# Kernel optimization log

Measured on AMD Instinct MI355X. Metric: run time of the kernel, lower is better.

Reference implementation:

```python
import jax, jax.numpy as jnp
import numpy as np

D_HEAD = 64
KV_GROUPS = 3
KSIZE = 7


def _win_idx(L, ksize):
    # NATTEN neighborhood: window centered at i, shifted to stay in-bounds.
    start = jnp.clip(jnp.arange(L) - ksize // 2, 0, L - ksize)  # [L]
    return start[:, None] + jnp.arange(ksize)[None, :]          # [L, k]


def _natten2d(q, k, v, ksize):
    # q,k,v: [n, nh, H, W, e]; q pre-scaled.
    H, W = q.shape[2], q.shape[3]
    ih = _win_idx(H, ksize)  # [H, k]
    iw = _win_idx(W, ksize)  # [W, k]
    # gather per-query key/value windows: [n, nh, H, W, k, k, e]
    kg = k[:, :, ih[:, None, :, None], iw[None, :, None, :], :]
    vg = v[:, :, ih[:, None, :, None], iw[None, :, None, :], :]
    logits = jnp.einsum('nhije,nhijabe->nhijab', q, kg)  # [n,nh,H,W,k,k]
    n_, nh = logits.shape[:2]
    a = jax.nn.softmax(logits.reshape(n_, nh, H, W, ksize * ksize), axis=-1)
    a = a.reshape(logits.shape)
    return jnp.einsum('nhijab,nhijabe->nhije', a, vg)  # [n,nh,H,W,e]


def _to_heads(p, nh, e):
    n, h, w, _ = p.shape
    return p.reshape(n, h, w, nh, e).transpose(0, 3, 1, 2, 4)  # [n,nh,h,w,e]


def setup_inputs() -> dict:
    key = jax.random.key(0)
    k1, k2, k3 = jax.random.split(key, 3)
    x = jax.random.normal(k1, (2, 32, 32, 768), dtype=jnp.float32)
    w_qkv = jax.random.normal(k2, (1280, 768), dtype=jnp.float32) * 0.02
    w_out = jax.random.normal(k3, (768, 768), dtype=jnp.float32) * 0.02
    return {"x": x, "w_qkv": w_qkv, "w_out": w_out}


def reference(x, w_qkv, w_out):
    n, H, W, d_model = x.shape
    q_heads = d_model // D_HEAD
    kv_heads = q_heads // KV_GROUPS
    qkv = x @ w_qkv.T  # [n,H,W,1280]
    q, k, v = jnp.split(
        qkv, [q_heads * D_HEAD, (q_heads + kv_heads) * D_HEAD], axis=-1)
    q = _to_heads(q, q_heads, D_HEAD)
    k = jnp.tile(_to_heads(k, kv_heads, D_HEAD), (1, KV_GROUPS, 1, 1, 1))
    v = jnp.tile(_to_heads(v, kv_heads, D_HEAD), (1, KV_GROUPS, 1, 1, 1))
    q = q / (D_HEAD ** 0.5)
    o = _natten2d(q, k, v, KSIZE)           # [n,nh,H,W,e]
    o = o.transpose(0, 2, 3, 1, 4).reshape(n, H, W, d_model)
    return o @ w_out.T
```

## Files before the change

kernel.cpp:

```cpp
#include <hip/hip_runtime.h>
#include <hip/hip_bf16.h>


typedef __attribute__((ext_vector_type(8))) __bf16 bf16x8;
typedef __attribute__((ext_vector_type(4))) float floatx4;
typedef unsigned short u16;

__device__ inline u16 f2bf(float f) {
    union { float f; unsigned u; } v; v.f = f;
    return (u16)((v.u + 0x7fff + ((v.u >> 16) & 1)) >> 16);
}

__device__ inline void gl_lds16(const void* g, void* l) {
    __builtin_amdgcn_global_load_lds(
        (const __attribute__((address_space(1))) void*)g,
        (__attribute__((address_space(3))) void*)l, 16, 0, 0);
}

__global__ __launch_bounds__(256) void convert_kernel(
    const float* __restrict__ x, const float* __restrict__ w1,
    const float* __restrict__ w2, u16* __restrict__ xb,
    u16* __restrict__ w1b, u16* __restrict__ w2b)
{
    int t = blockIdx.x * blockDim.x + threadIdx.x;
    const float* s; u16* d;
    if (t < 393216)      { s = x;  d = xb; }
    else if (t < 638976) { s = w1; d = w1b; t -= 393216; }
    else                 { s = w2; d = w2b; t -= 638976; }
    float4 v = ((const float4*)s)[t];
    ushort4 o;
    o.x = f2bf(v.x); o.y = f2bf(v.y); o.z = f2bf(v.z); o.w = f2bf(v.w);
    ((ushort4*)d)[t] = o;
}

template<int MODE>
__global__ __launch_bounds__(256) void gemm_nt(
    const u16* __restrict__ A, const u16* __restrict__ B,
    float* __restrict__ out, u16* __restrict__ Cq, u16* __restrict__ vT,
    int K)
{
    __shared__ __align__(16) u16 As[8 * 2048];
    __shared__ __align__(16) u16 Bs[8 * 2048];
    const int tid = threadIdx.x;
    const int lane = tid & 63;
    const int wave = tid >> 6;
    const int bm = blockIdx.y * 64;
    const int bn = blockIdx.x * 64;
    const int qr = (wave >> 1) * 32;
    const int qc = (wave & 1) * 32;

    floatx4 acc[2][2] = {};

    const u16* Xsrc = (wave < 2) ? A : B;
    const int   bx  = (wave < 2) ? bm : bn;
    u16* Xlds       = (wave < 2) ? As : Bs;
    const int half  = wave & 1;
    const int l2 = lane >> 2;
    const int l3 = (lane & 3) * 8;
    int gofs[16], lofs[16];
    #pragma unroll
    for (int cc = 0; cc < 16; cc++) {
        int c = half * 16 + cc, kc = c & 7, rg = c >> 3;
        gofs[cc] = (bx + rg * 16 + l2) * K + kc * 32 + l3;
        lofs[cc] = kc * 2048 + rg * 512;
    }

    const int fr = lane & 15;
    const int fk = (lane >> 4) * 8;

    for (int k0 = 0; k0 < K; k0 += 256) {
        #pragma unroll
        for (int cc = 0; cc < 16; cc++)
            gl_lds16(Xsrc + gofs[cc] + k0, Xlds + lofs[cc]);
        __syncthreads();
        #pragma unroll
        for (int kc = 0; kc < 8; kc++) {
            bf16x8 af0 = *(const bf16x8*)&As[kc * 2048 + (qr +      fr) * 32 + fk];
            bf16x8 af1 = *(const bf16x8*)&As[kc * 2048 + (qr + 16 + fr) * 32 + fk];
            bf16x8 bf0 = *(const bf16x8*)&Bs[kc * 2048 + (qc +      fr) * 32 + fk];
            bf16x8 bf1 = *(const bf16x8*)&Bs[kc * 2048 + (qc + 16 + fr) * 32 + fk];
            acc[0][0] = __builtin_amdgcn_mfma_f32_16x16x32_bf16(af0, bf0, acc[0][0], 0, 0, 0);
            acc[0][1] = __builtin_amdgcn_mfma_f32_16x16x32_bf16(af0, bf1, acc[0][1], 0, 0, 0);
            acc[1][0] = __builtin_amdgcn_mfma_f32_16x16x32_bf16(af1, bf0, acc[1][0], 0, 0, 0);
            acc[1][1] = __builtin_amdgcn_mfma_f32_16x16x32_bf16(af1, bf1, acc[1][1], 0, 0, 0);
        }
        __syncthreads();
    }

    const int cr = (lane >> 4) * 4;
    const int ccol = lane & 15;
    #pragma unroll
    for (int i = 0; i < 2; i++) {
        #pragma unroll
        for (int j = 0; j < 2; j++) {
            const int row0 = bm + qr + i * 16 + cr;
            const int col  = bn + qc + j * 16 + ccol;
            if (MODE == 0) {
                float4 w = {acc[i][j][0], acc[i][j][1], acc[i][j][2], acc[i][j][3]};
                *(float4*)&out[(size_t)col * 768 + row0] = w;
            } else {
                if (row0 < 1024) {
                    ushort4 w;
                    w.x = f2bf(acc[i][j][0]); w.y = f2bf(acc[i][j][1]);
                    w.z = f2bf(acc[i][j][2]); w.w = f2bf(acc[i][j][3]);
                    *(ushort4*)&Cq[(size_t)col * 1024 + row0] = w;
                } else {
                    #pragma unroll
                    for (int r = 0; r < 4; r++)
                        vT[(size_t)(row0 + r - 1024) * 2048 + col] = f2bf(acc[i][j][r]);
                }
            }
        }
    }
}

__global__ __launch_bounds__(256) void natten_mfma(
    const u16* __restrict__ qkv, const u16* __restrict__ vT,
    u16* __restrict__ o)
{
    __shared__ __align__(16) u16 Pw[4 * 512];
    const int h  = blockIdx.x;
    const int tb = blockIdx.y;
    const int g  = h & 3;
    const int batch = tb >> 4;
    const int ti = ((tb >> 2) & 3) * 8;
    const int tj = (tb & 3) * 8;
    const int wu_i = min(max(ti - 3, 0), 18);
    const int oj   = min(max(tj - 3, 0) & ~3, 16);
    const int lane = threadIdx.x & 63, wave = threadIdx.x >> 6;
    const int pixbase = batch << 10;

    const int fr = lane & 15;
    const int fk = (lane >> 4) * 8;

    bf16x8 aq0, aq1;
    {
        int qq = wave * 16 + fr;
        int pixq = pixbase + (ti + (qq >> 3)) * 32 + tj + (qq & 7);
        const u16* qp = &qkv[(size_t)pixq * 1024 + h * 64];
        aq0 = *(const bf16x8*)(qp + fk);
        aq1 = *(const bf16x8*)(qp + 32 + fk);
    }

    bool colok[4]; int tlo[4], thi[4];
    #pragma unroll
    for (int r = 0; r < 4; r++) {
        int qq = wave * 16 + (lane >> 4) * 4 + r;
        int qi = ti + (qq >> 3), qj = tj + (qq & 7);
        int si = min(max(qi - 3, 0), 25);
        int sj = min(max(qj - 3, 0), 25);
        colok[r] = (oj + fr >= sj) && (oj + fr <= sj + 6);
        tlo[r] = si - wu_i; thi[r] = tlo[r] + 6;
    }

    float s[14][4];
    float mx[4] = {-1e30f, -1e30f, -1e30f, -1e30f};
    #pragma unroll
    for (int t = 0; t < 14; t++) {
        int kp = pixbase + (wu_i + t) * 32 + oj + fr;
        const u16* krow = &qkv[(size_t)kp * 1024 + 768 + g * 64];
        bf16x8 bk0 = *(const bf16x8*)(krow + fk);
        bf16x8 bk1 = *(const bf16x8*)(krow + 32 + fk);
        floatx4 a4 = {};
        a4 = __builtin_amdgcn_mfma_f32_16x16x32_bf16(aq0, bk0, a4, 0, 0, 0);
        a4 = __builtin_amdgcn_mfma_f32_16x16x32_bf16(aq1, bk1, a4, 0, 0, 0);
        #pragma unroll
        for (int r = 0; r < 4; r++) {
            bool v = colok[r] && (t >= tlo[r]) && (t <= thi[r]);
            s[t][r] = v ? a4[r] * 0.125f : -1e30f;
            mx[r] = fmaxf(mx[r], s[t][r]);
        }
    }
    #pragma unroll
    for (int r = 0; r < 4; r++) {
        mx[r] = fmaxf(mx[r], __shfl_xor(mx[r], 1));
        mx[r] = fmaxf(mx[r], __shfl_xor(mx[r], 2));
        mx[r] = fmaxf(mx[r], __shfl_xor(mx[r], 4));
        mx[r] = fmaxf(mx[r], __shfl_xor(mx[r], 8));
    }
    float l[4] = {0.f, 0.f, 0.f, 0.f};
    #pragma unroll
    for (int t = 0; t < 14; t++)
        #pragma unroll
        for (int r = 0; r < 4; r++) {
            float p = __expf(s[t][r] - mx[r]);
            s[t][r] = p; l[r] += p;
        }
    #pragma unroll
    for (int r = 0; r < 4; r++) {
        l[r] += __shfl_xor(l[r], 1);
        l[r] += __shfl_xor(l[r], 2);
        l[r] += __shfl_xor(l[r], 4);
        l[r] += __shfl_xor(l[r], 8);
    }
    float rinv[4];
    #pragma unroll
    for (int r = 0; r < 4; r++) rinv[r] = 1.0f / l[r];

    u16* pw = &Pw[wave * 512];
    floatx4 oacc[4] = {};
    const int vrow = (fk >= 16) ? 1 : 0;
    const int vcol = oj + (fk & 8);
    #pragma unroll
    for (int kc = 0; kc < 7; kc++) {
        #pragma unroll
        for (int tt = 0; tt < 2; tt++) {
            int t = kc * 2 + tt;
            #pragma unroll
            for (int r = 0; r < 4; r++)
                pw[((lane >> 4) * 4 + r) * 32 + tt * 16 + fr] =
                    f2bf(s[t][r] * rinv[r]);
        }
        bf16x8 bp = *(const bf16x8*)&pw[fr * 32 + fk];
        const int vpix = pixbase + (wu_i + kc * 2 + vrow) * 32 + vcol;
        #pragma unroll
        for (int u = 0; u < 4; u++) {
            const u16* vp = &vT[(size_t)(g * 64 + u * 16 + fr) * 2048 + vpix];
            union { ushort4 q[2]; bf16x8 v; } av;
            av.q[0] = *(const ushort4*)vp;
            av.q[1] = *(const ushort4*)(vp + 4);
            oacc[u] = __builtin_amdgcn_mfma_f32_16x16x32_bf16(av.v, bp, oacc[u], 0, 0, 0);
        }
    }

    {
        int qq = wave * 16 + fr;
        int pixq = pixbase + (ti + (qq >> 3)) * 32 + tj + (qq & 7);
        u16* op = &o[(size_t)pixq * 768 + h * 64];
        #pragma unroll
        for (int u = 0; u < 4; u++) {
            ushort4 w;
            w.x = f2bf(oacc[u][0]); w.y = f2bf(oacc[u][1]);
            w.z = f2bf(oacc[u][2]); w.w = f2bf(oacc[u][3]);
            *(ushort4*)(op + u * 16 + (lane >> 4) * 4) = w;
        }
    }
}

extern "C" void kernel_launch(void* const* d_in, const int* in_sizes, int n_in,
                              void* d_out, int out_size, void* d_ws, size_t ws_size,
                              hipStream_t stream)
{
    const float* x     = (const float*)d_in[0];
    const float* w_qkv = (const float*)d_in[1];
    const float* w_out = (const float*)d_in[2];
    float* out = (float*)d_out;

    char* ws = (char*)d_ws;
    u16* qkvb = (u16*)ws; ws += (size_t)2048 * 1024 * 2;
    u16* vTb  = (u16*)ws; ws += (size_t)256 * 2048 * 2 + 64;
    u16* xb   = (u16*)ws; ws += (size_t)2048 * 768 * 2;
    u16* w1b  = (u16*)ws; ws += (size_t)1280 * 768 * 2;
    u16* w2b  = (u16*)ws; ws += (size_t)768 * 768 * 2;
    u16* ob   = (u16*)ws;

    convert_kernel<<<dim3(3072), dim3(256), 0, stream>>>(x, w_qkv, w_out, xb, w1b, w2b);

    gemm_nt<1><<<dim3(2048 / 64, 1280 / 64), dim3(256), 0, stream>>>(
        w1b, xb, nullptr, qkvb, vTb, 768);

    natten_mfma<<<dim3(12, 32), dim3(256), 0, stream>>>(qkvb, vTb, ob);

    gemm_nt<0><<<dim3(2048 / 64, 768 / 64), dim3(256), 0, stream>>>(
        w2b, ob, out, nullptr, nullptr, 768);
}
```

Before: 104.1 us.

## Double-buffer GEMM LDS tiles with prefetch and batch conversion work per thread

The GEMM main loop moves from a single 256-wide K tile per iteration to two 128-wide LDS buffers. The next tile is loaded asynchronously into LDS while MFMAs run on the current one, with explicit vmcnt waits and barriers. The intent is to hide global load latency that was previously serialized behind a barrier. Separately, the convert kernel now handles three float4 elements per thread with a third of the blocks, which trades some occupancy for less launch and indexing overhead.

```diff
diff --git a/kernel.cpp b/kernel.cpp
--- a/kernel.cpp
+++ b/kernel.cpp
@@ -22,15 +22,19 @@
     const float* __restrict__ w2, u16* __restrict__ xb,
     u16* __restrict__ w1b, u16* __restrict__ w2b)
 {
-    int t = blockIdx.x * blockDim.x + threadIdx.x;
-    const float* s; u16* d;
-    if (t < 393216)      { s = x;  d = xb; }
-    else if (t < 638976) { s = w1; d = w1b; t -= 393216; }
-    else                 { s = w2; d = w2b; t -= 638976; }
-    float4 v = ((const float4*)s)[t];
-    ushort4 o;
-    o.x = f2bf(v.x); o.y = f2bf(v.y); o.z = f2bf(v.z); o.w = f2bf(v.w);
-    ((ushort4*)d)[t] = o;
+    int t0 = blockIdx.x * 256 + threadIdx.x;
+    #pragma unroll
+    for (int rep = 0; rep < 3; rep++) {
+        int t = t0 + rep * 262144;
+        const float* s; u16* d; int i = t;
+        if (t < 393216)      { s = x;  d = xb; }
+        else if (t < 638976) { s = w1; d = w1b; i = t - 393216; }
+        else                 { s = w2; d = w2b; i = t - 638976; }
+        float4 v = ((const float4*)s)[i];
+        ushort4 o;
+        o.x = f2bf(v.x); o.y = f2bf(v.y); o.z = f2bf(v.z); o.w = f2bf(v.w);
+        ((ushort4*)d)[i] = o;
+    }
 }
 
 template<int MODE>
@@ -39,8 +43,8 @@
     float* __restrict__ out, u16* __restrict__ Cq, u16* __restrict__ vT,
     int K)
 {
-    __shared__ __align__(16) u16 As[8 * 2048];
-    __shared__ __align__(16) u16 Bs[8 * 2048];
+    __shared__ __align__(16) u16 As[2][4 * 2048];
+    __shared__ __align__(16) u16 Bs[2][4 * 2048];
     const int tid = threadIdx.x;
     const int lane = tid & 63;
     const int wave = tid >> 6;
@@ -51,16 +55,17 @@
 
     floatx4 acc[2][2] = {};
 
-    const u16* Xsrc = (wave < 2) ? A : B;
-    const int   bx  = (wave < 2) ? bm : bn;
-    u16* Xlds       = (wave < 2) ? As : Bs;
+    const bool isA  = (wave < 2);
+    const u16* Xsrc = isA ? A : B;
+    const int   bx  = isA ? bm : bn;
+    u16* Xbase      = isA ? &As[0][0] : &Bs[0][0];
     const int half  = wave & 1;
     const int l2 = lane >> 2;
     const int l3 = (lane & 3) * 8;
-    int gofs[16], lofs[16];
-    #pragma unroll
-    for (int cc = 0; cc < 16; cc++) {
-        int c = half * 16 + cc, kc = c & 7, rg = c >> 3;
+    int gofs[8], lofs[8];
+    #pragma unroll
+    for (int cc = 0; cc < 8; cc++) {
+        int c = half * 8 + cc, kc = c & 3, rg = c >> 2;
         gofs[cc] = (bx + rg * 16 + l2) * K + kc * 32 + l3;
         lofs[cc] = kc * 2048 + rg * 512;
     }
@@ -68,23 +73,39 @@
     const int fr = lane & 15;
     const int fk = (lane >> 4) * 8;
 
-    for (int k0 = 0; k0 < K; k0 += 256) {
-        #pragma unroll
-        for (int cc = 0; cc < 16; cc++)
-            gl_lds16(Xsrc + gofs[cc] + k0, Xlds + lofs[cc]);
-        __syncthreads();
-        #pragma unroll
-        for (int kc = 0; kc < 8; kc++) {
-            bf16x8 af0 = *(const bf16x8*)&As[kc * 2048 + (qr +      fr) * 32 + fk];
-            bf16x8 af1 = *(const bf16x8*)&As[kc * 2048 + (qr + 16 + fr) * 32 + fk];
-            bf16x8 bf0 = *(const bf16x8*)&Bs[kc * 2048 + (qc +      fr) * 32 + fk];
-            bf16x8 bf1 = *(const bf16x8*)&Bs[kc * 2048 + (qc + 16 + fr) * 32 + fk];
+    const int NIT = K >> 7;
+    int cur = 0;
+
+    #pragma unroll
+    for (int cc = 0; cc < 8; cc++)
+        gl_lds16(Xsrc + gofs[cc], Xbase + lofs[cc]);
+    asm volatile("s_waitcnt vmcnt(0)" ::: "memory");
+    __builtin_amdgcn_s_barrier();
+
+    for (int it = 0; it < NIT; ++it) {
+        if (it + 1 < NIT) {
+            u16* dst = Xbase + ((cur ^ 1) << 13);
+            const int k0 = (it + 1) << 7;
+            #pragma unroll
+            for (int cc = 0; cc < 8; cc++)
+                gl_lds16(Xsrc + gofs[cc] + k0, dst + lofs[cc]);
+        }
+        const u16* as = &As[0][0] + (cur << 13);
+        const u16* bs = &Bs[0][0] + (cur << 13);
+        #pragma unroll
+        for (int kc = 0; kc < 4; kc++) {
+            bf16x8 af0 = *(const bf16x8*)&as[kc * 2048 + (qr +      fr) * 32 + fk];
+            bf16x8 af1 = *(const bf16x8*)&as[kc * 2048 + (qr + 16 + fr) * 32 + fk];
+            bf16x8 bf0 = *(const bf16x8*)&bs[kc * 2048 + (qc +      fr) * 32 + fk];
+            bf16x8 bf1 = *(const bf16x8*)&bs[kc * 2048 + (qc + 16 + fr) * 32 + fk];
             acc[0][0] = __builtin_amdgcn_mfma_f32_16x16x32_bf16(af0, bf0, acc[0][0], 0, 0, 0);
             acc[0][1] = __builtin_amdgcn_mfma_f32_16x16x32_bf16(af0, bf1, acc[0][1], 0, 0, 0);
             acc[1][0] = __builtin_amdgcn_mfma_f32_16x16x32_bf16(af1, bf0, acc[1][0], 0, 0, 0);
             acc[1][1] = __builtin_amdgcn_mfma_f32_16x16x32_bf16(af1, bf1, acc[1][1], 0, 0, 0);
         }
-        __syncthreads();
+        asm volatile("s_waitcnt vmcnt(0)" ::: "memory");
+        __builtin_amdgcn_s_barrier();
+        cur ^= 1;
     }
 
     const int cr = (lane >> 4) * 4;
@@ -254,7 +275,7 @@
     u16* w2b  = (u16*)ws; ws += (size_t)768 * 768 * 2;
     u16* ob   = (u16*)ws;
 
-    convert_kernel<<<dim3(3072), dim3(256), 0, stream>>>(x, w_qkv, w_out, xb, w1b, w2b);
+    convert_kernel<<<dim3(1024), dim3(256), 0, stream>>>(x, w_qkv, w_out, xb, w1b, w2b);
 
     gemm_nt<1><<<dim3(2048 / 64, 1280 / 64), dim3(256), 0, stream>>>(
         w1b, xb, nullptr, qkvb, vTb, 768);
```

New measurement: 105.8 us. About the same (+1.6%).
